# Kernel tuning notes

Measured on AMD Instinct MI355X. Metric: run time of the kernel, lower is better.

Reference implementation:

```python
import jax, jax.numpy as jnp
import numpy as np

NUM_GROUPS = 32
EPS = 1e-5


def setup_inputs() -> dict:
    key = jax.random.key(0)
    ks = jax.random.split(key, 4)
    B, C, H, W = 4, 256, 64, 64
    x = jax.random.normal(ks[0], (B, C, H, W), dtype=jnp.float32)
    norm_w = jnp.ones((C,), dtype=jnp.float32)
    norm_b = jnp.zeros((C,), dtype=jnp.float32)
    qkv_w = jax.random.normal(ks[1], (3 * C, C), dtype=jnp.float32) * (C ** -0.5)
    qkv_b = jnp.zeros((3 * C,), dtype=jnp.float32)
    proj_w = jax.random.normal(ks[2], (C, C), dtype=jnp.float32) * (C ** -0.5)
    proj_b = jnp.zeros((C,), dtype=jnp.float32)
    return {"x": x, "norm_w": norm_w, "norm_b": norm_b, "qkv_w": qkv_w,
            "qkv_b": qkv_b, "proj_w": proj_w, "proj_b": proj_b, "num_heads": 1}


def _group_norm(x, w, b):
    B, C, H, W = x.shape
    xg = x.reshape(B, NUM_GROUPS, C // NUM_GROUPS, H, W)
    mean = xg.mean(axis=(2, 3, 4), keepdims=True)
    var = xg.var(axis=(2, 3, 4), keepdims=True)
    xn = ((xg - mean) * jax.lax.rsqrt(var + EPS)).reshape(B, C, H, W)
    return xn * w[None, :, None, None] + b[None, :, None, None]


def reference(x, norm_w, norm_b, qkv_w, qkv_b, proj_w, proj_b, num_heads):
    B, C, H, W = x.shape
    N = H * W
    d = C // num_heads
    xn = _group_norm(x, norm_w, norm_b)
    # 1x1 conv == channel matmul: [B,3C,H,W]
    qkv = jnp.einsum('oc,bchw->bohw', qkv_w, xn) + qkv_b[None, :, None, None]
    qkv = qkv.reshape(B, 3, num_heads, d, N)
    q, k, v = qkv[:, 0], qkv[:, 1], qkv[:, 2]  # each [B,h,d,N]
    scale = d ** -0.5
    attn = jnp.einsum('bhdi,bhdj->bhij', q, k) * scale  # [B,h,N,N]
    attn = jax.nn.softmax(attn, axis=-1)
    out = jnp.einsum('bhij,bhdj->bhdi', attn, v)  # [B,h,d,N]
    out = out.reshape(B, C, H, W)
    out = jnp.einsum('oc,bchw->bohw', proj_w, out) + proj_b[None, :, None, None]
    return x + out
```

## Files before the change

kernel.cpp:

```cpp
#include <hip/hip_runtime.h>
#include <stdint.h>
#include <stddef.h>

#define NB 4
#define NC 256
#define NSP 4096
#define NG 32
#define CPG 8
#define GEPS 1e-5f
#define SCALE 0.0625f
#define NROWS (NB * NSP)
#define JSPLIT 4

typedef __attribute__((ext_vector_type(8))) short s8v;
typedef __attribute__((ext_vector_type(4))) float f4v;
typedef __attribute__((ext_vector_type(16))) float f16v;
typedef __attribute__((ext_vector_type(4))) unsigned short us4v;
typedef __attribute__((ext_vector_type(4))) unsigned int u4v;

__device__ __forceinline__ float b2f(unsigned short h) {
  union { unsigned u; float f; } x; x.u = ((unsigned)h) << 16; return x.f;
}
__device__ __forceinline__ unsigned short f2b(float f) {
  union { float f; unsigned u; } x; x.f = f;
  unsigned r = x.u + 0x7fffu + ((x.u >> 16) & 1u);
  return (unsigned short)(r >> 16);
}
__device__ __forceinline__ unsigned packbf(float lo, float hi) {
  union { float f; unsigned u; } a, b; a.f = lo; b.f = hi;
  return (b.u & 0xffff0000u) | (a.u >> 16);
}
__device__ __forceinline__ s8v pack8(float4 lo, float4 hi) {
  s8v r;
  ((unsigned short*)&r)[0] = f2b(lo.x);
  ((unsigned short*)&r)[1] = f2b(lo.y);
  ((unsigned short*)&r)[2] = f2b(lo.z);
  ((unsigned short*)&r)[3] = f2b(lo.w);
  ((unsigned short*)&r)[4] = f2b(hi.x);
  ((unsigned short*)&r)[5] = f2b(hi.y);
  ((unsigned short*)&r)[6] = f2b(hi.z);
  ((unsigned short*)&r)[7] = f2b(hi.w);
  return r;
}

__global__ __launch_bounds__(512) void gn_kernel(
    const float* __restrict__ x, const float* __restrict__ w,
    const float* __restrict__ bias, unsigned short* __restrict__ xn) {
  int b = blockIdx.x >> 5;
  int g = blockIdx.x & 31;
  const float* xp = x + ((size_t)b * NC + (size_t)g * CPG) * NSP;
  int t = threadIdx.x;

  __shared__ float xs[CPG * NSP];
  __shared__ float r1[512], r2[512];

  float s = 0.f, ss = 0.f;
  for (int i = 4 * t; i < CPG * NSP; i += 2048) {
    float4 v = *(const float4*)(xp + i);
    *(float4*)(xs + i) = v;
    s += v.x + v.y + v.z + v.w;
    ss += v.x * v.x + v.y * v.y + v.z * v.z + v.w * v.w;
  }
  r1[t] = s; r2[t] = ss;
  __syncthreads();
  for (int off = 256; off > 0; off >>= 1) {
    if (t < off) { r1[t] += r1[t + off]; r2[t] += r2[t + off]; }
    __syncthreads();
  }
  float mean = r1[0] * (1.f / (CPG * NSP));
  float var  = r2[0] * (1.f / (CPG * NSP)) - mean * mean;
  float rstd = rsqrtf(var + GEPS);
  float wv[CPG], bv[CPG];
  for (int c = 0; c < CPG; c++) {
    wv[c] = w[g * CPG + c] * rstd;
    bv[c] = bias[g * CPG + c] - mean * wv[c];
  }
  for (int n = t; n < NSP; n += 512) {
    s8v pk;
    for (int c = 0; c < CPG; c++) {
      float v = xs[c * NSP + n];
      ((unsigned short*)&pk)[c] = f2b(v * wv[c] + bv[c]);
    }
    *(s8v*)(xn + ((size_t)(b * NSP + n) * NC + g * CPG)) = pk;
  }
}

__global__ __launch_bounds__(256) void qkv_gemm(
    const float* __restrict__ Wf, const unsigned short* __restrict__ xnG,
    const float* __restrict__ qkvb,
    unsigned short* __restrict__ q, unsigned short* __restrict__ k,
    unsigned short* __restrict__ v) {
  const int sec = blockIdx.y >> 1;
  const int m0 = (blockIdx.y & 1) * 128;
  const int n0 = blockIdx.x * 128;
  const float* A = Wf + (size_t)sec * NC * NC;
  const unsigned short* Bt = xnG + (size_t)blockIdx.z * NSP * NC;
  unsigned short* dst = (sec == 0 ? q : (sec == 1 ? k : v)) + (size_t)blockIdx.z * NSP * NC;
  const float scl = (sec == 0) ? SCALE : 1.f;

  __shared__ unsigned short S[8192];
  unsigned short* As = S;
  unsigned short* Bs = S + 4096;
  const int t = threadIdx.x;
  const int lane = t & 63, wave = t >> 6;
  const int wm = (wave >> 1) * 64, wn = (wave & 1) * 64;
  const int l16 = lane & 15, quad = lane >> 4;
  const int srow = t >> 2, skc = (t & 3) * 8;

  f4v acc[4][4];
  for (int mi = 0; mi < 4; mi++)
    for (int ni = 0; ni < 4; ni++)
      acc[mi][ni] = (f4v){0.f, 0.f, 0.f, 0.f};

  const float* Ag0 = A + (size_t)(m0 + srow) * NC + skc;
  const float* Ag1 = A + (size_t)(m0 + srow + 64) * NC + skc;
  const unsigned short* Bg0 = Bt + (size_t)(n0 + srow) * NC + skc;
  const unsigned short* Bg1 = Bt + (size_t)(n0 + srow + 64) * NC + skc;

  for (int k0 = 0; k0 < NC; k0 += 32) {
    s8v a0 = pack8(*(const float4*)(Ag0 + k0), *(const float4*)(Ag0 + k0 + 4));
    s8v a1 = pack8(*(const float4*)(Ag1 + k0), *(const float4*)(Ag1 + k0 + 4));
    s8v b0 = *(const s8v*)(Bg0 + k0);
    s8v b1 = *(const s8v*)(Bg1 + k0);
    __syncthreads();
    *(s8v*)(As + srow * 32 + skc) = a0;
    *(s8v*)(As + (srow + 64) * 32 + skc) = a1;
    *(s8v*)(Bs + srow * 32 + skc) = b0;
    *(s8v*)(Bs + (srow + 64) * 32 + skc) = b1;
    __syncthreads();
    s8v af[4], bfr[4];
    for (int mi = 0; mi < 4; mi++)
      af[mi] = *(const s8v*)(As + (wm + mi * 16 + l16) * 32 + quad * 8);
    for (int ni = 0; ni < 4; ni++)
      bfr[ni] = *(const s8v*)(Bs + (wn + ni * 16 + l16) * 32 + quad * 8);
    for (int mi = 0; mi < 4; mi++)
      for (int ni = 0; ni < 4; ni++)
        acc[mi][ni] = __builtin_amdgcn_mfma_f32_16x16x32_bf16(af[mi], bfr[ni], acc[mi][ni], 0, 0, 0);
  }

  if (sec < 2) {
    for (int mi = 0; mi < 4; mi++) {
      const int rb = m0 + wm + mi * 16 + quad * 4;
      for (int ni = 0; ni < 4; ni++) {
        const int col = n0 + wn + ni * 16 + l16;
        f4v a = acc[mi][ni];
        unsigned short pk[4];
        for (int r = 0; r < 4; r++)
          pk[r] = f2b((a[r] + qkvb[sec * NC + rb + r]) * scl);
        unsigned w0 = (unsigned)pk[0] | ((unsigned)pk[1] << 16);
        unsigned w1 = (unsigned)pk[2] | ((unsigned)pk[3] << 16);
        unsigned p0 = __shfl_xor(w0, 16, 64);
        unsigned p1 = __shfl_xor(w1, 16, 64);
        if (!(quad & 1)) {
          u4v full; full[0] = w0; full[1] = w1; full[2] = p0; full[3] = p1;
          const size_t off = (size_t)(col >> 5) * 8192 + (rb >> 4) * 512 +
                             ((rb >> 3) & 1) * 256 + (col & 31) * 8;
          *(s8v*)(dst + off) = __builtin_bit_cast(s8v, full);
        }
      }
    }
  } else {
    for (int h = 0; h < 2; h++) {
      __syncthreads();
      for (int mi = 0; mi < 4; mi++) {
        const int dlb = wm + mi * 16 + quad * 4;
        for (int nn = 0; nn < 2; nn++) {
          const int ni = 2 * h + nn;
          const int jl = wn + ni * 16 + l16;
          f4v a = acc[mi][ni];
          const int base = ((jl >> 6) & 1) * 4096 + ((jl >> 3) & 3) * 256 + (jl & 7);
          for (int r = 0; r < 4; r++) {
            const int dl = dlb + r;
            S[base + (dl >> 5) * 1024 + (dl & 31) * 8] =
                f2b(a[r] + qkvb[2 * NC + m0 + dl]);
          }
        }
      }
      __syncthreads();
      for (int i = 0; i < 4; i++) {
        const int c = i * 256 + t;
        const int jtbit = c >> 9;
        const int dgrp = (c >> 7) & 3;
        const int rest = (c & 127) * 8;
        unsigned short* gdst = dst + (size_t)(n0 / 32 + 2 * jtbit + h) * 8192 +
                               (size_t)(m0 / 32 + dgrp) * 1024 + rest;
        *(s8v*)gdst = *(const s8v*)(S + c * 8);
      }
    }
  }
}

__global__ __launch_bounds__(256, 2) void flash12_kernel(
    const unsigned short* __restrict__ q, const unsigned short* __restrict__ k,
    const unsigned short* __restrict__ v, unsigned short* __restrict__ Opart,
    float* __restrict__ Lpart) {
  const int qt = blockIdx.x, b = blockIdx.y, js = blockIdx.z;
  const size_t sNC = (size_t)NSP * NC;
  const unsigned short* qb = q + b * sNC;
  const unsigned short* kb = k + b * sNC;
  const unsigned short* vb = v + b * sNC;
  const int t = threadIdx.x, lane = t & 63, w = t >> 6;

  __shared__ unsigned short K_lds[2][16 * 512];
  __shared__ unsigned short V_lds[2][16 * 512];

  f16v zero16;
  #pragma unroll
  for (int r = 0; r < 16; r++) zero16[r] = 0.f;

  s8v qf[16];
  {
    const unsigned short* qp = qb + (size_t)(qt * 4 + w) * 8192 + lane * 8;
    #pragma unroll
    for (int kc = 0; kc < 16; kc++)
      qf[kc] = *(const s8v*)(qp + kc * 512);
  }

  f16v accO[8];
  #pragma unroll
  for (int dt = 0; dt < 8; dt++) accO[dt] = zero16;
  float l4[4] = {0.f, 0.f, 0.f, 0.f};

  const int jbeg = js * (NSP / JSPLIT);
  const int NT = (NSP / JSPLIT) / 32;

  auto stage = [&](int j0, int bufsel) {
    const size_t tb = (size_t)(j0 >> 5) * 16;
    #pragma unroll
    for (int ii = 0; ii < 8; ii++) {
      const int idx = w * 8 + ii;
      const unsigned short* gp;
      unsigned short* ld;
      if (idx < 16) {
        gp = kb + (tb + idx) * 512 + lane * 8;
        ld = &K_lds[bufsel][idx * 512];
      } else {
        const int dt = idx - 16;
        gp = vb + (tb + dt) * 512 + lane * 8;
        ld = &V_lds[bufsel][dt * 512];
      }
      __builtin_amdgcn_global_load_lds(
          (const __attribute__((address_space(1))) unsigned int*)gp,
          (__attribute__((address_space(3))) unsigned int*)ld, 16, 0, 0);
    }
  };

  stage(jbeg, 0);
  for (int jt = 0; jt < NT; jt++) {
    __syncthreads();
    if (jt + 1 < NT) stage(jbeg + (jt + 1) * 32, (jt + 1) & 1);
    const unsigned short* Kc = K_lds[jt & 1];
    const unsigned short* Vc = V_lds[jt & 1];

    f16v accS = zero16;
    #pragma unroll
    for (int kc = 0; kc < 16; kc++) {
      s8v kf = *(const s8v*)(Kc + kc * 512 + lane * 8);
      accS = __builtin_amdgcn_mfma_f32_32x32x16_bf16(kf, qf[kc], accS, 0, 0, 0);
    }

    float p[16];
    #pragma unroll
    for (int r = 0; r < 16; r++) {
      p[r] = __expf(accS[r]);
      l4[r & 3] += p[r];
    }

    u4v pw0, pw1;
    {
      unsigned a0 = packbf(p[0], p[1]),   b0 = packbf(p[4], p[5]);
      asm("v_permlane32_swap_b32 %0, %1" : "+v"(a0), "+v"(b0));
      unsigned a1 = packbf(p[2], p[3]),   b1 = packbf(p[6], p[7]);
      asm("v_permlane32_swap_b32 %0, %1" : "+v"(a1), "+v"(b1));
      unsigned a2 = packbf(p[8], p[9]),   b2 = packbf(p[12], p[13]);
      asm("v_permlane32_swap_b32 %0, %1" : "+v"(a2), "+v"(b2));
      unsigned a3 = packbf(p[10], p[11]), b3 = packbf(p[14], p[15]);
      asm("v_permlane32_swap_b32 %0, %1" : "+v"(a3), "+v"(b3));
      pw0[0] = a0; pw0[1] = a1; pw0[2] = b0; pw0[3] = b1;
      pw1[0] = a2; pw1[1] = a3; pw1[2] = b2; pw1[3] = b3;
    }
    const s8v pb0 = __builtin_bit_cast(s8v, pw0);
    const s8v pb1 = __builtin_bit_cast(s8v, pw1);

    #pragma unroll
    for (int dt = 0; dt < 8; dt++) {
      s8v vf0 = *(const s8v*)(Vc + dt * 1024 + lane * 8);
      s8v vf1 = *(const s8v*)(Vc + dt * 1024 + 512 + lane * 8);
      accO[dt] = __builtin_amdgcn_mfma_f32_32x32x16_bf16(vf0, pb0, accO[dt], 0, 0, 0);
      accO[dt] = __builtin_amdgcn_mfma_f32_32x32x16_bf16(vf1, pb1, accO[dt], 0, 0, 0);
    }
  }

  float l_acc = l4[0] + l4[1] + l4[2] + l4[3];
  const float ltot = l_acc + __shfl_xor(l_acc, 32, 64);
  const int qrow = b * NSP + qt * 128 + w * 32 + (lane & 31);
  if (lane < 32)
    Lpart[(size_t)js * NROWS + qrow] = ltot;

  unsigned short* Op = Opart + ((size_t)js * NROWS + qrow) * NC;
  const int hi = lane >> 5;
  #pragma unroll
  for (int dt = 0; dt < 8; dt++) {
    #pragma unroll
    for (int g = 0; g < 4; g++) {
      unsigned short pk[4];
      #pragma unroll
      for (int r = 0; r < 4; r++)
        pk[r] = f2b(accO[dt][g * 4 + r]);
      unsigned w0 = (unsigned)pk[0] | ((unsigned)pk[1] << 16);
      unsigned w1 = (unsigned)pk[2] | ((unsigned)pk[3] << 16);
      unsigned p0 = __shfl_xor(w0, 32, 64);
      unsigned p1 = __shfl_xor(w1, 32, 64);
      if (hi == 0) {
        u4v full; full[0] = w0; full[1] = w1; full[2] = p0; full[3] = p1;
        *(s8v*)(Op + dt * 32 + g * 8) = __builtin_bit_cast(s8v, full);
      }
    }
  }
}

__global__ __launch_bounds__(256) void proj_gemm(
    const float* __restrict__ Wpf, const unsigned short* __restrict__ Opart,
    const float* __restrict__ Lpart, const float* __restrict__ pb,
    const float* __restrict__ x, float* __restrict__ out) {
  const int z = blockIdx.z, m0 = blockIdx.y * 128, n0 = blockIdx.x * 128;
  __shared__ unsigned short As[128 * 32], Bs[128 * 32];
  const int t = threadIdx.x;
  const int lane = t & 63, wave = t >> 6;
  const int wm = (wave >> 1) * 64, wn = (wave & 1) * 64;
  const int l16 = lane & 15, quad = lane >> 4;
  const int srow = t >> 2, skc = (t & 3) * 8;

  const int prow0 = z * NSP + n0 + srow;
  const int prow1 = prow0 + 64;
  float ls0 = 0.f, ls1 = 0.f;
  for (int js = 0; js < JSPLIT; js++) {
    ls0 += Lpart[(size_t)js * NROWS + prow0];
    ls1 += Lpart[(size_t)js * NROWS + prow1];
  }
  const float inv0 = 1.f / ls0, inv1 = 1.f / ls1;

  f4v acc[4][4];
  for (int mi = 0; mi < 4; mi++)
    for (int ni = 0; ni < 4; ni++)
      acc[mi][ni] = (f4v){0.f, 0.f, 0.f, 0.f};

  const float* Ag0 = Wpf + (size_t)(m0 + srow) * NC + skc;
  const float* Ag1 = Wpf + (size_t)(m0 + srow + 64) * NC + skc;

  for (int k0 = 0; k0 < NC; k0 += 32) {
    s8v a0 = pack8(*(const float4*)(Ag0 + k0), *(const float4*)(Ag0 + k0 + 4));
    s8v a1 = pack8(*(const float4*)(Ag1 + k0), *(const float4*)(Ag1 + k0 + 4));
    float bv0[8], bv1[8];
    for (int e = 0; e < 8; e++) { bv0[e] = 0.f; bv1[e] = 0.f; }
    for (int js = 0; js < JSPLIT; js++) {
      const s8v o0 = *(const s8v*)(Opart + ((size_t)js * NROWS + prow0) * NC + k0 + skc);
      const s8v o1 = *(const s8v*)(Opart + ((size_t)js * NROWS + prow1) * NC + k0 + skc);
      for (int e = 0; e < 8; e++) {
        bv0[e] += b2f(((const unsigned short*)&o0)[e]);
        bv1[e] += b2f(((const unsigned short*)&o1)[e]);
      }
    }
    s8v b0, b1;
    for (int e = 0; e < 8; e++) {
      ((unsigned short*)&b0)[e] = f2b(bv0[e] * inv0);
      ((unsigned short*)&b1)[e] = f2b(bv1[e] * inv1);
    }
    __syncthreads();
    *(s8v*)(As + srow * 32 + skc) = a0;
    *(s8v*)(As + (srow + 64) * 32 + skc) = a1;
    *(s8v*)(Bs + srow * 32 + skc) = b0;
    *(s8v*)(Bs + (srow + 64) * 32 + skc) = b1;
    __syncthreads();
    s8v af[4], bfr[4];
    for (int mi = 0; mi < 4; mi++)
      af[mi] = *(const s8v*)(As + (wm + mi * 16 + l16) * 32 + quad * 8);
    for (int ni = 0; ni < 4; ni++)
      bfr[ni] = *(const s8v*)(Bs + (wn + ni * 16 + l16) * 32 + quad * 8);
    for (int mi = 0; mi < 4; mi++)
      for (int ni = 0; ni < 4; ni++)
        acc[mi][ni] = __builtin_amdgcn_mfma_f32_16x16x32_bf16(af[mi], bfr[ni], acc[mi][ni], 0, 0, 0);
  }

  float* C = out + (size_t)z * NC * NSP;
  const float* R = x + (size_t)z * NC * NSP;
  for (int mi = 0; mi < 4; mi++) {
    const int rb = m0 + wm + mi * 16 + quad * 4;
    for (int ni = 0; ni < 4; ni++) {
      const int col = n0 + wn + ni * 16 + l16;
      f4v a = acc[mi][ni];
      for (int r = 0; r < 4; r++)
        C[(size_t)(rb + r) * NSP + col] =
            a[r] + pb[rb + r] + R[(size_t)(rb + r) * NSP + col];
    }
  }
}

extern "C" void kernel_launch(void* const* d_in, const int* in_sizes, int n_in,
                              void* d_out, int out_size, void* d_ws, size_t ws_size,
                              hipStream_t stream) {
  const float* x      = (const float*)d_in[0];
  const float* norm_w = (const float*)d_in[1];
  const float* norm_b = (const float*)d_in[2];
  const float* qkv_w  = (const float*)d_in[3];
  const float* qkv_b  = (const float*)d_in[4];
  const float* proj_w = (const float*)d_in[5];
  const float* proj_b = (const float*)d_in[6];
  float* out = (float*)d_out;

  char* ws = (char*)d_ws;
  char* wst = ws + (1 << 20);
  const size_t szBNC = (size_t)NB * NSP * NC * 2;
  unsigned short* xn = (unsigned short*)wst;
  unsigned short* q  = (unsigned short*)(wst + szBNC);
  unsigned short* k  = (unsigned short*)(wst + 2 * szBNC);
  unsigned short* v  = (unsigned short*)(wst + 3 * szBNC);
  unsigned short* Opart = (unsigned short*)(wst + 4 * szBNC);
  float* Lpart = (float*)(wst + 4 * szBNC + (size_t)JSPLIT * NROWS * NC * 2);

  gn_kernel<<<dim3(NB * NG), 512, 0, stream>>>(x, norm_w, norm_b, xn);
  qkv_gemm<<<dim3(NSP / 128, 6, NB), 256, 0, stream>>>(qkv_w, xn, qkv_b, q, k, v);
  flash12_kernel<<<dim3(NSP / 128, NB, JSPLIT), 256, 0, stream>>>(q, k, v, Opart, Lpart);
  proj_gemm<<<dim3(NSP / 128, NC / 128, NB), 256, 0, stream>>>(
      proj_w, Opart, Lpart, proj_b, x, out);
}
```

Baseline: 207.3 us.

## Fold split-K partial sum into proj GEMM K-loop with async LDS staging

The projection GEMM no longer sums the JSPLIT attention partials in registers before the MMA. It treats the four partials as an extended K dimension of 1024 and stages them directly into double-buffered LDS with global_load_lds. The 1/l normalisation is applied per column in the epilogue, and the whole proj weight tile is preloaded into padded LDS once. The flash kernel's output store also drops the cross-lane shuffle in favour of direct 8-byte stores, at the cost of four times more MFMA work in the proj GEMM.

```diff
diff --git a/kernel.cpp b/kernel.cpp
--- a/kernel.cpp
+++ b/kernel.cpp
@@ -11,6 +11,7 @@
 #define SCALE 0.0625f
 #define NROWS (NB * NSP)
 #define JSPLIT 4
+#define ALD 264
 
 typedef __attribute__((ext_vector_type(8))) short s8v;
 typedef __attribute__((ext_vector_type(4))) float f4v;
@@ -190,7 +191,7 @@
   }
 }
 
-__global__ __launch_bounds__(256, 2) void flash12_kernel(
+__global__ __launch_bounds__(256, 2) void flash13_kernel(
     const unsigned short* __restrict__ q, const unsigned short* __restrict__ k,
     const unsigned short* __restrict__ v, unsigned short* __restrict__ Opart,
     float* __restrict__ Lpart) {
@@ -303,18 +304,11 @@
   for (int dt = 0; dt < 8; dt++) {
     #pragma unroll
     for (int g = 0; g < 4; g++) {
-      unsigned short pk[4];
+      us4v pk;
       #pragma unroll
       for (int r = 0; r < 4; r++)
         pk[r] = f2b(accO[dt][g * 4 + r]);
-      unsigned w0 = (unsigned)pk[0] | ((unsigned)pk[1] << 16);
-      unsigned w1 = (unsigned)pk[2] | ((unsigned)pk[3] << 16);
-      unsigned p0 = __shfl_xor(w0, 32, 64);
-      unsigned p1 = __shfl_xor(w1, 32, 64);
-      if (hi == 0) {
-        u4v full; full[0] = w0; full[1] = w1; full[2] = p0; full[3] = p1;
-        *(s8v*)(Op + dt * 32 + g * 8) = __builtin_bit_cast(s8v, full);
-      }
+      *(us4v*)(Op + dt * 32 + g * 8 + hi * 4) = pk;
     }
   }
 }
@@ -324,59 +318,62 @@
     const float* __restrict__ Lpart, const float* __restrict__ pb,
     const float* __restrict__ x, float* __restrict__ out) {
   const int z = blockIdx.z, m0 = blockIdx.y * 128, n0 = blockIdx.x * 128;
-  __shared__ unsigned short As[128 * 32], Bs[128 * 32];
+  __shared__ unsigned short Asf[128 * ALD];
+  __shared__ unsigned short Bsd[2][128 * 32];
   const int t = threadIdx.x;
   const int lane = t & 63, wave = t >> 6;
   const int wm = (wave >> 1) * 64, wn = (wave & 1) * 64;
   const int l16 = lane & 15, quad = lane >> 4;
   const int srow = t >> 2, skc = (t & 3) * 8;
 
-  const int prow0 = z * NSP + n0 + srow;
-  const int prow1 = prow0 + 64;
-  float ls0 = 0.f, ls1 = 0.f;
-  for (int js = 0; js < JSPLIT; js++) {
-    ls0 += Lpart[(size_t)js * NROWS + prow0];
-    ls1 += Lpart[(size_t)js * NROWS + prow1];
-  }
-  const float inv0 = 1.f / ls0, inv1 = 1.f / ls1;
+  for (int i = 0; i < 16; i++) {
+    const int idx = i * 256 + t;
+    const int row = idx >> 5;
+    const int cc = (idx & 31) * 8;
+    const float* src = Wpf + (size_t)(m0 + row) * NC + cc;
+    *(s8v*)(Asf + row * ALD + cc) = pack8(*(const float4*)src, *(const float4*)(src + 4));
+  }
+
+  float inv[4];
+  for (int ni = 0; ni < 4; ni++) {
+    const int col = n0 + wn + ni * 16 + l16;
+    float ls = 0.f;
+    for (int js = 0; js < JSPLIT; js++)
+      ls += Lpart[(size_t)js * NROWS + z * NSP + col];
+    inv[ni] = 1.f / ls;
+  }
 
   f4v acc[4][4];
   for (int mi = 0; mi < 4; mi++)
     for (int ni = 0; ni < 4; ni++)
       acc[mi][ni] = (f4v){0.f, 0.f, 0.f, 0.f};
 
-  const float* Ag0 = Wpf + (size_t)(m0 + srow) * NC + skc;
-  const float* Ag1 = Wpf + (size_t)(m0 + srow + 64) * NC + skc;
-
-  for (int k0 = 0; k0 < NC; k0 += 32) {
-    s8v a0 = pack8(*(const float4*)(Ag0 + k0), *(const float4*)(Ag0 + k0 + 4));
-    s8v a1 = pack8(*(const float4*)(Ag1 + k0), *(const float4*)(Ag1 + k0 + 4));
-    float bv0[8], bv1[8];
-    for (int e = 0; e < 8; e++) { bv0[e] = 0.f; bv1[e] = 0.f; }
-    for (int js = 0; js < JSPLIT; js++) {
-      const s8v o0 = *(const s8v*)(Opart + ((size_t)js * NROWS + prow0) * NC + k0 + skc);
-      const s8v o1 = *(const s8v*)(Opart + ((size_t)js * NROWS + prow1) * NC + k0 + skc);
-      for (int e = 0; e < 8; e++) {
-        bv0[e] += b2f(((const unsigned short*)&o0)[e]);
-        bv1[e] += b2f(((const unsigned short*)&o1)[e]);
-      }
-    }
-    s8v b0, b1;
-    for (int e = 0; e < 8; e++) {
-      ((unsigned short*)&b0)[e] = f2b(bv0[e] * inv0);
-      ((unsigned short*)&b1)[e] = f2b(bv1[e] * inv1);
-    }
+  auto stageB = [&](int kk, int bufsel) {
+    const int js = kk >> 3, c0 = (kk & 7) * 32;
+    const unsigned short* g0 =
+        Opart + ((size_t)js * NROWS + z * NSP + n0 + srow) * NC + c0 + skc;
+    __builtin_amdgcn_global_load_lds(
+        (const __attribute__((address_space(1))) unsigned int*)g0,
+        (__attribute__((address_space(3))) unsigned int*)(Bsd[bufsel] + srow * 32 + skc),
+        16, 0, 0);
+    const unsigned short* g1 = g0 + (size_t)64 * NC;
+    __builtin_amdgcn_global_load_lds(
+        (const __attribute__((address_space(1))) unsigned int*)g1,
+        (__attribute__((address_space(3))) unsigned int*)(Bsd[bufsel] + (srow + 64) * 32 + skc),
+        16, 0, 0);
+  };
+
+  stageB(0, 0);
+  for (int kk = 0; kk < 32; kk++) {
     __syncthreads();
-    *(s8v*)(As + srow * 32 + skc) = a0;
-    *(s8v*)(As + (srow + 64) * 32 + skc) = a1;
-    *(s8v*)(Bs + srow * 32 + skc) = b0;
-    *(s8v*)(Bs + (srow + 64) * 32 + skc) = b1;
-    __syncthreads();
+    if (kk + 1 < 32) stageB(kk + 1, (kk + 1) & 1);
+    const unsigned short* Bc = Bsd[kk & 1];
+    const int c0 = (kk & 7) * 32;
     s8v af[4], bfr[4];
     for (int mi = 0; mi < 4; mi++)
-      af[mi] = *(const s8v*)(As + (wm + mi * 16 + l16) * 32 + quad * 8);
+      af[mi] = *(const s8v*)(Asf + (wm + mi * 16 + l16) * ALD + c0 + quad * 8);
     for (int ni = 0; ni < 4; ni++)
-      bfr[ni] = *(const s8v*)(Bs + (wn + ni * 16 + l16) * 32 + quad * 8);
+      bfr[ni] = *(const s8v*)(Bc + (wn + ni * 16 + l16) * 32 + quad * 8);
     for (int mi = 0; mi < 4; mi++)
       for (int ni = 0; ni < 4; ni++)
         acc[mi][ni] = __builtin_amdgcn_mfma_f32_16x16x32_bf16(af[mi], bfr[ni], acc[mi][ni], 0, 0, 0);
@@ -391,7 +388,7 @@
       f4v a = acc[mi][ni];
       for (int r = 0; r < 4; r++)
         C[(size_t)(rb + r) * NSP + col] =
-            a[r] + pb[rb + r] + R[(size_t)(rb + r) * NSP + col];
+            a[r] * inv[ni] + pb[rb + r] + R[(size_t)(rb + r) * NSP + col];
     }
   }
 }
@@ -420,7 +417,7 @@
 
   gn_kernel<<<dim3(NB * NG), 512, 0, stream>>>(x, norm_w, norm_b, xn);
   qkv_gemm<<<dim3(NSP / 128, 6, NB), 256, 0, stream>>>(qkv_w, xn, qkv_b, q, k, v);
-  flash12_kernel<<<dim3(NSP / 128, NB, JSPLIT), 256, 0, stream>>>(q, k, v, Opart, Lpart);
+  flash13_kernel<<<dim3(NSP / 128, NB, JSPLIT), 256, 0, stream>>>(q, k, v, Opart, Lpart);
   proj_gemm<<<dim3(NSP / 128, NC / 128, NB), 256, 0, stream>>>(
       proj_w, Opart, Lpart, proj_b, x, out);
 }
```

Result: no change. 207.5 us (+0.1%).
